# Performance work log

Hardware: AMD Instinct MI355X
Metric: run time of the kernel (lower is better)

## Reference

```python
import jax, jax.numpy as jnp
import numpy as np

N_NODES = 100000

def _sage_conv(x, edge_index, W_l, b_l, W_r):
    # PyG SAGEConv default: mean-aggregate neighbor (source) features at dst,
    # then out = lin_l(agg) + lin_r(x). lin_l has bias, lin_r does not.
    src, dst = edge_index[0], edge_index[1]
    msg = x[src]                                   # [E, F]
    summed = jax.ops.segment_sum(msg, dst, num_segments=N_NODES)  # [N, F]
    cnt = jax.ops.segment_sum(jnp.ones((src.shape[0],), x.dtype), dst,
                              num_segments=N_NODES)
    agg = summed / jnp.maximum(cnt, 1.0)[:, None]
    return agg @ W_l + b_l + x @ W_r


def setup_inputs() -> dict:
    key = jax.random.key(0)
    ks = jax.random.split(key, 10)
    F_IN, H, C = 128, 16, 8
    E = 3200000
    x = jax.random.normal(ks[0], (N_NODES, F_IN), dtype=jnp.float32)
    edge_index = jax.random.randint(ks[1], (2, E), 0, N_NODES, dtype=jnp.int64)
    s1 = 1.0 / np.sqrt(F_IN)
    s2 = 1.0 / np.sqrt(H)
    sc = 1.0 / np.sqrt(2 * H)
    return {
        "x": x,
        "edge_index": edge_index,
        "W1_l": jax.random.uniform(ks[2], (F_IN, H), jnp.float32, -s1, s1),
        "b1": jnp.zeros((H,), jnp.float32),
        "W1_r": jax.random.uniform(ks[3], (F_IN, H), jnp.float32, -s1, s1),
        "W2_l": jax.random.uniform(ks[4], (H, H), jnp.float32, -s2, s2),
        "b2": jnp.zeros((H,), jnp.float32),
        "W2_r": jax.random.uniform(ks[5], (H, H), jnp.float32, -s2, s2),
        "Wc": jax.random.uniform(ks[6], (2 * H, C), jnp.float32, -sc, sc),
        "bc": jax.random.uniform(ks[7], (C,), jnp.float32, -sc, sc),
    }


def reference(x, edge_index, W1_l, b1, W1_r, W2_l, b2, W2_r, Wc, bc):
    h = jax.nn.relu(_sage_conv(x, edge_index, W1_l, b1, W1_r))
    # F.dropout(training=False) in eval mode -> identity
    h = jax.nn.relu(_sage_conv(h, edge_index, W2_l, b2, W2_r))
    edge_feat = jnp.concatenate([h[edge_index[0]], h[edge_index[1]]], axis=-1)  # [E, 32]
    logits = edge_feat @ Wc + bc                                                # [E, C]
    return jax.nn.log_softmax(logits, axis=1)
```

## Files before the change

### kernel.cpp

```cpp
#include <hip/hip_runtime.h>
#include <hip/hip_bf16.h>
#include <hip/hip_fp16.h>


#define NBLK 256
#define BUCKET_BITS 8
#define BUCKET_SZ 256
#define CAP 9216
#define MAXNB 512

struct __align__(16) H8 { __half2 a, b, c, d; };

__global__ __launch_bounds__(512) void prep_kernel(const int* __restrict__ ei,
                                                   int* __restrict__ gcur,
                                                   int* __restrict__ elist,
                                                   const float* __restrict__ x,
                                                   const float* __restrict__ W1l,
                                                   const float* __restrict__ W1r,
                                                   __half* __restrict__ yh,
                                                   __half* __restrict__ zh,
                                                   int E, int N, int NB, int chunk,
                                                   int nbin) {
  __shared__ float smem[64 * 129 + 128 * 32];
  int t = threadIdx.x;
  if ((int)blockIdx.x < nbin) {
    int* hist = (int*)smem;
    int* cur  = hist + MAXNB;
    for (int i = t; i < NB; i += 512) hist[i] = 0;
    __syncthreads();
    int s = blockIdx.x * chunk;
    int eend = s + chunk; if (eend > E) eend = E;
    for (int e = s + t; e < eend; e += 512)
      atomicAdd(&hist[ei[E + e] >> BUCKET_BITS], 1);
    __syncthreads();
    for (int i = t; i < NB; i += 512) {
      int c = hist[i];
      cur[i] = i * CAP + (c ? atomicAdd(&gcur[i], c) : 0);
    }
    __syncthreads();
    for (int e = s + t; e < eend; e += 512) {
      int src = ei[e];
      int dst = ei[E + e];
      int b = dst >> BUCKET_BITS;
      int pos = atomicAdd(&cur[b], 1);
      elist[pos] = ((dst & (BUCKET_SZ - 1)) << 17) | src;
    }
  } else {
    float* Xs = smem;
    float* Ws = smem + 64 * 129;
    int nb = ((int)blockIdx.x - nbin) * 64;
    for (int i = t; i < 128 * 16; i += 512) {
      int kk = i >> 4, c = i & 15;
      Ws[kk * 32 + c] = W1l[i];
      Ws[kk * 32 + 16 + c] = W1r[i];
    }
    const float4* xg = (const float4*)(x + (size_t)nb * 128);
    for (int i4 = t; i4 < 64 * 32; i4 += 512) {
      int r = i4 >> 5, c4 = (i4 & 31) * 4;
      float4 val = make_float4(0.f, 0.f, 0.f, 0.f);
      if (nb + r < N) val = xg[i4];
      float* dp = &Xs[r * 129 + c4];
      dp[0] = val.x; dp[1] = val.y; dp[2] = val.z; dp[3] = val.w;
    }
    __syncthreads();
    int n = t & 63, cg = t >> 6;
    float a0 = 0.f, a1 = 0.f, a2 = 0.f, a3 = 0.f;
    for (int kk = 0; kk < 128; ++kk) {
      float xv = Xs[n * 129 + kk];
      const float* wr = &Ws[kk * 32 + cg * 4];
      a0 += xv * wr[0]; a1 += xv * wr[1]; a2 += xv * wr[2]; a3 += xv * wr[3];
    }
    int node = nb + n;
    if (node < N) {
      int c = cg * 4;
      __half2 h01 = __floats2half2_rn(a0, a1);
      __half2 h23 = __floats2half2_rn(a2, a3);
      if (c < 16) {
        __half2* yp = (__half2*)(yh + (size_t)node * 16 + c);
        yp[0] = h01; yp[1] = h23;
      } else {
        __half2* zp = (__half2*)(zh + (size_t)node * 16 + (c - 16));
        zp[0] = h01; zp[1] = h23;
      }
    }
  }
}

__global__ __launch_bounds__(512) void sortagg_kernel(int* __restrict__ elist,
                                                      const int* __restrict__ gcur,
                                                      int* __restrict__ row_csr,
                                                      int* __restrict__ row_end,
                                                      const __half* __restrict__ yh,
                                                      const __half* __restrict__ zh,
                                                      const float* __restrict__ b1,
                                                      const float* __restrict__ W2l,
                                                      const float* __restrict__ W2r,
                                                      __half* __restrict__ ph,
                                                      __half* __restrict__ qh, int N) {
  extern __shared__ int sm[];
  int* sorted = sm;
  int* hist   = sm + CAP;
  int* wtmp   = hist + 256;
  float* Wl_s = (float*)(wtmp + 4);
  float* Wr_s = Wl_s + 256;
  float* b_s  = Wr_s + 256;
  int t = threadIdx.x;
  int b = blockIdx.x;
  int lane = t & 63, wid = t >> 6;
  if (t < 256) { Wl_s[t] = W2l[t]; Wr_s[t] = W2r[t]; hist[t] = 0; }
  else if (t < 272) b_s[t - 256] = b1[t - 256];
  int beg = b * CAP;
  int cnt = gcur[b];
  if (cnt > CAP) cnt = CAP;
  __syncthreads();
  for (int i = t; i < cnt; i += 512)
    atomicAdd(&hist[((unsigned)elist[beg + i]) >> 17], 1);
  __syncthreads();
  {
    int v = (t < 256) ? hist[t] : 0;
    int incl = v;
#pragma unroll
    for (int d = 1; d < 64; d <<= 1) {
      int u = __shfl_up(incl, d);
      if (lane >= d) incl += u;
    }
    if (t < 256 && lane == 63) wtmp[wid] = incl;
    __syncthreads();
    if (t < 64) {
      int w = (t < 4) ? wtmp[t] : 0;
#pragma unroll
      for (int d = 1; d < 4; d <<= 1) {
        int u = __shfl_up(w, d);
        if (lane >= d) w += u;
      }
      if (t < 4) wtmp[t] = w;
    }
    __syncthreads();
    if (t < 256) {
      int excl = ((wid > 0) ? wtmp[wid - 1] : 0) + (incl - v);
      hist[t] = excl;
      int node = (b << BUCKET_BITS) + t;
      if (node < N) row_csr[node] = beg + excl;
    }
  }
  __syncthreads();
  for (int i = t; i < cnt; i += 512) {
    unsigned ent = (unsigned)elist[beg + i];
    int pos = atomicAdd(&hist[ent >> 17], 1);
    sorted[pos] = ent & 0x1FFFF;
  }
  __syncthreads();
  if (t < 256) {
    int node = (b << BUCKET_BITS) + t;
    if (node < N) row_end[node] = beg + hist[t];
  }
  for (int i = t; i < cnt; i += 512) elist[beg + i] = sorted[i];
  const __half2* yh2 = (const __half2*)yh;
  int base = b << BUCKET_BITS;
  int k = t & 7;
#pragma unroll
  for (int pass = 0; pass < 4; ++pass) {
    int dl = pass * 64 + (t >> 3);
    int node = base + dl;
    if (node < N) {
      int rbeg = dl ? hist[dl - 1] : 0;
      int rend = hist[dl];
      float a0 = 0.f, a1 = 0.f;
      int j = rbeg;
      for (; j + 4 <= rend; j += 4) {
        int s0 = sorted[j], s1 = sorted[j + 1];
        int s2 = sorted[j + 2], s3 = sorted[j + 3];
        float2 v0 = __half22float2(yh2[(size_t)s0 * 8 + k]);
        float2 v1 = __half22float2(yh2[(size_t)s1 * 8 + k]);
        float2 v2 = __half22float2(yh2[(size_t)s2 * 8 + k]);
        float2 v3 = __half22float2(yh2[(size_t)s3 * 8 + k]);
        a0 += v0.x + v1.x + v2.x + v3.x;
        a1 += v0.y + v1.y + v2.y + v3.y;
      }
      for (; j < rend; ++j) {
        float2 v = __half22float2(yh2[(size_t)sorted[j] * 8 + k]);
        a0 += v.x; a1 += v.y;
      }
      int deg = rend - rbeg;
      float inv = 1.f / (float)(deg > 0 ? deg : 1);
      float2 zv = __half22float2(((const __half2*)zh)[(size_t)node * 8 + k]);
      float h0 = fmaxf(a0 * inv + b_s[2 * k]     + zv.x, 0.f);
      float h1 = fmaxf(a1 * inv + b_s[2 * k + 1] + zv.y, 0.f);
      float pa0 = 0.f, pa1 = 0.f, qa0 = 0.f, qa1 = 0.f;
      int c0 = 2 * k;
#pragma unroll
      for (int kk2 = 0; kk2 < 8; ++kk2) {
        float ha = __shfl(h0, kk2, 8);
        float hb = __shfl(h1, kk2, 8);
        int r0 = 2 * kk2 * 16, r1 = r0 + 16;
        pa0 += ha * Wl_s[r0 + c0]     + hb * Wl_s[r1 + c0];
        pa1 += ha * Wl_s[r0 + c0 + 1] + hb * Wl_s[r1 + c0 + 1];
        qa0 += ha * Wr_s[r0 + c0]     + hb * Wr_s[r1 + c0];
        qa1 += ha * Wr_s[r0 + c0 + 1] + hb * Wr_s[r1 + c0 + 1];
      }
      ((__half2*)ph)[(size_t)node * 8 + k] = __floats2half2_rn(pa0, pa1);
      ((__half2*)qh)[(size_t)node * 8 + k] = __floats2half2_rn(qa0, qa1);
    }
  }
}

__global__ __launch_bounds__(256) void agg2_kernel(const __half* __restrict__ ph,
                                                   const __half* __restrict__ qh,
                                                   const int* __restrict__ row_csr,
                                                   const int* __restrict__ row_end,
                                                   const int* __restrict__ srclist,
                                                   const float* __restrict__ b2,
                                                   const float* __restrict__ Wc,
                                                   __half* __restrict__ Uh,
                                                   __half* __restrict__ Vh, int N) {
  __shared__ float Wc_s[256], b_s[16];
  int t = threadIdx.x;
  if (t < 256) Wc_s[t] = Wc[t];
  if (t < 16) b_s[t] = b2[t];
  __syncthreads();
  int g = (blockIdx.x * 256 + t) >> 3;
  int k = t & 7;
  if (g >= N) return;
  int beg = row_csr[g], end = row_end[g];
  const __half2* ph2 = (const __half2*)ph;
  float a0 = 0.f, a1 = 0.f;
  int j = beg;
  for (; j + 4 <= end; j += 4) {
    int s0 = srclist[j], s1 = srclist[j + 1];
    int s2 = srclist[j + 2], s3 = srclist[j + 3];
    float2 v0 = __half22float2(ph2[(size_t)s0 * 8 + k]);
    float2 v1 = __half22float2(ph2[(size_t)s1 * 8 + k]);
    float2 v2 = __half22float2(ph2[(size_t)s2 * 8 + k]);
    float2 v3 = __half22float2(ph2[(size_t)s3 * 8 + k]);
    a0 += v0.x + v1.x + v2.x + v3.x;
    a1 += v0.y + v1.y + v2.y + v3.y;
  }
  for (; j < end; ++j) {
    float2 v = __half22float2(ph2[(size_t)srclist[j] * 8 + k]);
    a0 += v.x; a1 += v.y;
  }
  int deg = end - beg;
  float inv = 1.f / (float)(deg > 0 ? deg : 1);
  float2 qv = __half22float2(((const __half2*)qh)[(size_t)g * 8 + k]);
  float h0 = fmaxf(a0 * inv + b_s[2 * k]     + qv.x, 0.f);
  float h1 = fmaxf(a1 * inv + b_s[2 * k + 1] + qv.y, 0.f);
  int wb = (k < 4) ? 0 : 128;
  int c0 = 2 * (k & 3);
  float o0 = 0.f, o1 = 0.f;
#pragma unroll
  for (int kk2 = 0; kk2 < 8; ++kk2) {
    float ha = __shfl(h0, kk2, 8);
    float hb = __shfl(h1, kk2, 8);
    int r0 = wb + 2 * kk2 * 8, r1 = r0 + 8;
    o0 += ha * Wc_s[r0 + c0]     + hb * Wc_s[r1 + c0];
    o1 += ha * Wc_s[r0 + c0 + 1] + hb * Wc_s[r1 + c0 + 1];
  }
  __half2 o = __floats2half2_rn(o0, o1);
  if (k < 4) ((__half2*)Uh)[(size_t)g * 4 + k] = o;
  else       ((__half2*)Vh)[(size_t)g * 4 + (k - 4)] = o;
}

#define EIL 4
__global__ __launch_bounds__(256) void edge_out_kernel(const int* __restrict__ ei,
                                                       const __half* __restrict__ Uh,
                                                       const __half* __restrict__ Vh,
                                                       const float* __restrict__ bc,
                                                       float* __restrict__ out, int E) {
  int base = blockIdx.x * (256 * EIL) + threadIdx.x;
  float4 c0 = ((const float4*)bc)[0], c1 = ((const float4*)bc)[1];
  int s[EIL], d[EIL];
#pragma unroll
  for (int ii = 0; ii < EIL; ++ii) {
    int e = base + ii * 256;
    s[ii] = (e < E) ? __builtin_nontemporal_load(ei + e) : 0;
    d[ii] = (e < E) ? __builtin_nontemporal_load(ei + E + e) : 0;
  }
  H8 u8[EIL], v8[EIL];
#pragma unroll
  for (int ii = 0; ii < EIL; ++ii) {
    u8[ii] = *(const H8*)(Uh + (size_t)s[ii] * 8);
    v8[ii] = *(const H8*)(Vh + (size_t)d[ii] * 8);
  }
#pragma unroll
  for (int ii = 0; ii < EIL; ++ii) {
    int e = base + ii * 256;
    if (e >= E) continue;
    float2 ua = __half22float2(u8[ii].a), ub = __half22float2(u8[ii].b);
    float2 uc = __half22float2(u8[ii].c), ud = __half22float2(u8[ii].d);
    float2 va = __half22float2(v8[ii].a), vb = __half22float2(v8[ii].b);
    float2 vc = __half22float2(v8[ii].c), vd = __half22float2(v8[ii].d);
    float tv[8];
    tv[0] = ua.x + va.x + c0.x; tv[1] = ua.y + va.y + c0.y;
    tv[2] = ub.x + vb.x + c0.z; tv[3] = ub.y + vb.y + c0.w;
    tv[4] = uc.x + vc.x + c1.x; tv[5] = uc.y + vc.y + c1.y;
    tv[6] = ud.x + vd.x + c1.z; tv[7] = ud.y + vd.y + c1.w;
    float m = tv[0];
#pragma unroll
    for (int c = 1; c < 8; ++c) m = fmaxf(m, tv[c]);
    float ssum = 0.f;
#pragma unroll
    for (int c = 0; c < 8; ++c) ssum += __expf(tv[c] - m);
    float lse = m + __logf(ssum);
    float4 o0 = make_float4(tv[0] - lse, tv[1] - lse, tv[2] - lse, tv[3] - lse);
    float4 o1 = make_float4(tv[4] - lse, tv[5] - lse, tv[6] - lse, tv[7] - lse);
    float4* op = (float4*)(out + (size_t)e * 8);
    op[0] = o0; op[1] = o1;
  }
}

extern "C" void kernel_launch(void* const* d_in, const int* in_sizes, int n_in,
                              void* d_out, int out_size, void* d_ws, size_t ws_size,
                              hipStream_t stream) {
  const float* x   = (const float*)d_in[0];
  const int*   ei  = (const int*)d_in[1];
  const float* W1l = (const float*)d_in[2];
  const float* b1  = (const float*)d_in[3];
  const float* W1r = (const float*)d_in[4];
  const float* W2l = (const float*)d_in[5];
  const float* b2  = (const float*)d_in[6];
  const float* W2r = (const float*)d_in[7];
  const float* Wc  = (const float*)d_in[8];
  const float* bc  = (const float*)d_in[9];
  float* out = (float*)d_out;

  const int N = in_sizes[0] / 128;
  const int E = in_sizes[1] / 2;
  const size_t N16 = (size_t)N * 16;
  const int NB = (N + BUCKET_SZ - 1) >> BUCKET_BITS;
  const int chunk = (E + NBLK - 1) / NBLK;

  __half* yh = (__half*)d_ws;
  __half* ph = yh + N16;
  __half* zh = ph + N16;
  __half* qh = zh + N16;
  __half* Uh = qh + N16;
  __half* Vh = Uh + (size_t)N * 8;
  int* gcur    = (int*)(Vh + (size_t)N * 8);
  int* elist   = gcur + NB;
  int* row_csr = elist + (size_t)NB * CAP;
  int* row_end = row_csr + N;

  hipMemsetAsync(gcur, 0, NB * sizeof(int), stream);

  int lin1_blocks = (N + 63) / 64;
  prep_kernel<<<NBLK + lin1_blocks, 512, 0, stream>>>(ei, gcur, elist, x, W1l,
                                                      W1r, yh, zh, E, N, NB,
                                                      chunk, NBLK);

  size_t smem = (CAP + 256 + 4) * sizeof(int) + 528 * sizeof(float);
  sortagg_kernel<<<NB, 512, smem, stream>>>(elist, gcur, row_csr, row_end,
                                            yh, zh, b1, W2l, W2r, ph, qh, N);

  int ngrid = (N * 8 + 255) / 256;
  agg2_kernel<<<ngrid, 256, 0, stream>>>(ph, qh, row_csr, row_end, elist,
                                         b2, Wc, Uh, Vh, N);

  int egrid = (E + 256 * EIL - 1) / (256 * EIL);
  edge_out_kernel<<<egrid, 256, 0, stream>>>(ei, Uh, Vh, bc, out, E);
}
```

Baseline: 184.2 us.

## Stage bucketed edges in shared memory before coalesced global scatter

The binning blocks now run a block-wide prefix scan over the bucket histogram. Each edge is scattered into a shared-memory staging buffer sorted by bucket, and the staged entries are then written to global memory in contiguous runs, with each entry's bucket found by binary search. This replaces scattered per-edge global writes with mostly coalesced ones. The block count rises to 320 so each chunk fits the shared staging buffer, at the cost of an extra scan, extra syncs and a per-element binary search.

New measurement: 170.3 us, median of 2. 7.6% less time.

```diff
diff --git a/kernel.cpp b/kernel.cpp
--- a/kernel.cpp
+++ b/kernel.cpp
@@ -3,11 +3,12 @@
 #include <hip/hip_fp16.h>
 
 
-#define NBLK 256
+#define NBLK 320
 #define BUCKET_BITS 8
 #define BUCKET_SZ 256
 #define CAP 9216
 #define MAXNB 512
+#define CHUNK_MAX 10240
 
 struct __align__(16) H8 { __half2 a, b, c, d; };
 
@@ -24,26 +25,64 @@
   __shared__ float smem[64 * 129 + 128 * 32];
   int t = threadIdx.x;
   if ((int)blockIdx.x < nbin) {
-    int* hist = (int*)smem;
-    int* cur  = hist + MAXNB;
+    int* hist  = (int*)smem;
+    int* loc   = hist + MAXNB;
+    int* gbase = loc + MAXNB;
+    int* wtmp  = gbase + MAXNB;
+    int* stage = wtmp + 8;
+    int lane = t & 63, wid = t >> 6;
     for (int i = t; i < NB; i += 512) hist[i] = 0;
     __syncthreads();
     int s = blockIdx.x * chunk;
     int eend = s + chunk; if (eend > E) eend = E;
+    int cnt = eend - s;
     for (int e = s + t; e < eend; e += 512)
       atomicAdd(&hist[ei[E + e] >> BUCKET_BITS], 1);
     __syncthreads();
-    for (int i = t; i < NB; i += 512) {
-      int c = hist[i];
-      cur[i] = i * CAP + (c ? atomicAdd(&gcur[i], c) : 0);
+    {
+      int v = (t < NB) ? hist[t] : 0;
+      int incl = v;
+#pragma unroll
+      for (int d = 1; d < 64; d <<= 1) {
+        int u = __shfl_up(incl, d);
+        if (lane >= d) incl += u;
+      }
+      if (lane == 63) wtmp[wid] = incl;
+      __syncthreads();
+      if (t < 64) {
+        int w = (t < 8) ? wtmp[t] : 0;
+#pragma unroll
+        for (int d = 1; d < 8; d <<= 1) {
+          int u = __shfl_up(w, d);
+          if (lane >= d) w += u;
+        }
+        if (t < 8) wtmp[t] = w;
+      }
+      __syncthreads();
+      if (t < NB) {
+        int excl = ((wid > 0) ? wtmp[wid - 1] : 0) + (incl - v);
+        loc[t] = excl;
+        gbase[t] = t * CAP + (v ? atomicAdd(&gcur[t], v) : 0);
+        hist[t] = excl;
+      }
     }
     __syncthreads();
     for (int e = s + t; e < eend; e += 512) {
       int src = ei[e];
       int dst = ei[E + e];
       int b = dst >> BUCKET_BITS;
-      int pos = atomicAdd(&cur[b], 1);
-      elist[pos] = ((dst & (BUCKET_SZ - 1)) << 17) | src;
+      int pos = atomicAdd(&hist[b], 1);
+      stage[pos] = ((dst & (BUCKET_SZ - 1)) << 17) | src;
+    }
+    __syncthreads();
+    for (int i = t; i < cnt; i += 512) {
+      int lo = 0, hi = NB;
+#pragma unroll 9
+      while (hi - lo > 1) {
+        int mid = (lo + hi) >> 1;
+        if (loc[mid] <= i) lo = mid; else hi = mid;
+      }
+      elist[gbase[lo] + (i - loc[lo])] = stage[i];
     }
   } else {
     float* Xs = smem;
```
